# Performance work log

Measured on AMD Instinct MI355X. Metric: run time of the kernel, lower is better.

## Reference

```python
import jax, jax.numpy as jnp
from jax import lax
import numpy as np

GRID = 64
MAP = 15000.0
SCALE = MAP / GRID  # 234.375
R = int(1100 / SCALE)  # 4
SIGMA = 1.5
C = 16
B = 768
N_KILL = 49152
N_TRAIL = 393216

TOWERS = np.array([(8955, 8510), (9767, 10113), (11134, 11207), (11593, 11669), (13052, 12612), (12611, 13084), (5846, 6396), (5048, 4812), (3651, 3696), (3210, 3217), (2177, 1807), (1748, 2270), (4318, 13875), (981, 10441), (7943, 13411), (1512, 6699), (1169, 4287), (1172, 3583), (10481, 13650), (11275, 13657), (11275, 13663), (13866, 4505), (10504, 1029), (13327, 8226), (13624, 10572), (6919, 1483), (13599, 11319), (4281, 1253), (3468, 1230), (13594, 11319)], dtype=np.float32)

# ---- static buffers (numpy, computed once at import) ----
_tg = np.clip((TOWERS / SCALE).astype(np.int64), 0, GRID - 1)
TX, TY = _tg[:, 0], _tg[:, 1]
_xs = np.arange(GRID)
# per-tower coverage disc on the full canvas: equivalent to clipped range_mask placement
DISC = (((_xs[None, None, :] - TX[:, None, None]) ** 2 + (_xs[None, :, None] - TY[:, None, None]) ** 2) <= R * R).astype(np.float32)  # [30, H, W]
_ks = int(2 * 4 * SIGMA + 1)
if _ks % 2 == 0:
    _ks += 1
_x = (np.arange(_ks) - _ks // 2).astype(np.float32)
_k1 = np.exp(-_x ** 2 / (2 * SIGMA ** 2))
_k2 = np.outer(_k1, _k1)
_k2 = _k2 / _k2.sum()
KERNEL = np.broadcast_to(_k2, (C, 1, _ks, _ks)).astype(np.float32).copy()  # depthwise OIHW
PAD = _ks // 2
DRAG_X, DRAG_Y = int(10000.0 / SCALE), int(5000.0 / SCALE)   # (42, 21)
BARON_X, BARON_Y = int(5000.0 / SCALE), int(10000.0 / SCALE)  # (21, 42)


def _to_grid(coords):
    return jnp.clip((coords / SCALE).astype(jnp.int32), 0, GRID - 1)


def setup_inputs() -> dict:
    key = jax.random.key(0)
    ks = jax.random.split(key, 10)
    return {
        "player_coords": jax.random.uniform(ks[0], (N_TRAIL, 2), jnp.float32) * MAP,
        "player_vals": jax.random.uniform(ks[1], (N_TRAIL,), jnp.float32),
        "dead_towers_mask": jax.random.uniform(ks[2], (B, 30), jnp.float32),
        "kill_coords": jax.random.uniform(ks[3], (N_KILL, 2), jnp.float32) * MAP,
        "kill_vals": jax.random.uniform(ks[4], (N_KILL,), jnp.float32),
        "obj_status": jax.random.uniform(ks[5], (B, 2), jnp.float32),
        "player_b_idx": jax.random.randint(ks[6], (N_TRAIL,), 0, B, jnp.int32),
        "player_channels": jax.random.randint(ks[7], (N_TRAIL,), 0, 10, jnp.int32),
        "kill_teams": jax.random.randint(ks[8], (N_KILL,), 0, 2, jnp.int32),
        "kill_b_idx": jax.random.randint(ks[9], (N_KILL,), 0, B, jnp.int32),
    }


def reference(player_coords, player_vals, dead_towers_mask, kill_coords, kill_vals, obj_status, player_b_idx, player_channels, kill_teams, kill_b_idx):
    b = dead_towers_mask.shape[0]
    dead = dead_towers_mask > 0.5          # [B, 30]
    alive_f = (~dead).astype(jnp.float32)
    dead_f = dead.astype(jnp.float32)

    # channels 0/1: alive/dead tower markers (idempotent set -> scatter-max)
    ch0 = jnp.zeros((b, GRID, GRID), jnp.float32).at[:, TY, TX].max(alive_f)
    ch1 = jnp.zeros((b, GRID, GRID), jnp.float32).at[:, TY, TX].max(dead_f)

    # channel 2: max of binary range discs over alive towers == any-coverage indicator
    cov = alive_f @ jnp.asarray(DISC).reshape(30, -1)  # [B, H*W]
    ch2 = (cov > 0).astype(jnp.float32).reshape(b, GRID, GRID)

    # channel 3: objective markers
    ch3 = (jnp.zeros((b, GRID, GRID), jnp.float32)
           .at[:, DRAG_Y, DRAG_X].set((obj_status[:, 0] > 0.5).astype(jnp.float32))
           .at[:, BARON_Y, BARON_X].set((obj_status[:, 1] > 0.5).astype(jnp.float32)))

    canvas = jnp.concatenate(
        [ch0[:, None], ch1[:, None], ch2[:, None], ch3[:, None],
         jnp.zeros((b, C - 4, GRID, GRID), jnp.float32)], axis=1)  # [B, 16, H, W]

    # kill events: scatter-add into channels 4 + team
    kg = _to_grid(kill_coords)
    canvas = canvas.at[kill_b_idx, 4 + kill_teams, kg[:, 1], kg[:, 0]].add(kill_vals)

    # player trails: scatter-add into channels 6 + player_channel
    pg = _to_grid(player_coords)
    canvas = canvas.at[player_b_idx, 6 + player_channels, pg[:, 1], pg[:, 0]].add(player_vals)

    # depthwise gaussian blur
    blurred = lax.conv_general_dilated(
        canvas, jnp.asarray(KERNEL),
        window_strides=(1, 1), padding=[(PAD, PAD), (PAD, PAD)],
        feature_group_count=C,
        dimension_numbers=("NCHW", "OIHW", "NCHW"))
    return blurred
```

## Files before the change

### kernel.cpp

```cpp
#include <hip/hip_runtime.h>

#define GRID    64
#define BATCH   768
#define C       16
#define NT      30
#define N_KILL  49152
#define N_TRAIL 393216
#define CELLS   4096
#define IMG     (C * CELLS)
#define SCALE   234.375f
#define NBIN    (BATCH * 12)
#define STRIDE  65

__device__ constexpr int TX[NT] = {38,41,47,49,55,53,24,21,15,13, 9, 7,18, 4,33, 6, 4, 5,44,48,48,59,44,56,58,29,58,18,14,58};
__device__ constexpr int TY[NT] = {36,43,47,49,53,55,27,20,15,13, 7, 9,59,44,57,28,18,15,58,58,58,19, 4,35,45, 6,48, 5, 5,48};

__global__ __launch_bounds__(256) void zero_counts(unsigned* __restrict__ counts) {
    const int gid = blockIdx.x * 256 + threadIdx.x;
    if (gid < NBIN) counts[gid] = 0;
}

__global__ __launch_bounds__(256) void bin_points(
    const float* __restrict__ kc, const float* __restrict__ kv,
    const int*   __restrict__ kt, const int*   __restrict__ kb,
    const float* __restrict__ pc, const float* __restrict__ pv,
    const int*   __restrict__ pb, const int*   __restrict__ pch,
    unsigned* __restrict__ counts, uint2* __restrict__ recs, int cap)
{
    const int gid = blockIdx.x * 256 + threadIdx.x;
    int bin, cell; float val;
    if (gid < N_KILL) {
        const int i = gid;
        const int gx = min(max((int)(kc[2*i]   / SCALE), 0), GRID - 1);
        const int gy = min(max((int)(kc[2*i+1] / SCALE), 0), GRID - 1);
        cell = gy * GRID + gx;
        val  = kv[i];
        bin  = kb[i] * 12 + kt[i];
    } else {
        const int i = gid - N_KILL;
        const int gx = min(max((int)(pc[2*i]   / SCALE), 0), GRID - 1);
        const int gy = min(max((int)(pc[2*i+1] / SCALE), 0), GRID - 1);
        cell = gy * GRID + gx;
        val  = pv[i];
        bin  = pb[i] * 12 + 2 + pch[i];
    }
    const unsigned slot = atomicAdd(&counts[bin], 1u);
    if (slot < (unsigned)cap)
        recs[(size_t)bin * cap + slot] = make_uint2((unsigned)cell, __float_as_uint(val));
}

__global__ __launch_bounds__(256) void zero12(float* __restrict__ out) {
    const int j = blockIdx.x;
    const int b = j / 12, ch = 4 + j % 12;
    float4* p = (float4*)(out + (size_t)(b * C + ch) * CELLS);
    #pragma unroll
    for (int k = 0; k < 4; ++k) p[k * 256 + threadIdx.x] = make_float4(0.f,0.f,0.f,0.f);
}

__global__ __launch_bounds__(256) void scatter_global(
    const float* __restrict__ kc, const float* __restrict__ kv,
    const int*   __restrict__ kt, const int*   __restrict__ kb,
    const float* __restrict__ pc, const float* __restrict__ pv,
    const int*   __restrict__ pb, const int*   __restrict__ pch,
    float* __restrict__ out)
{
    const int gid = blockIdx.x * 256 + threadIdx.x;
    if (gid < N_KILL) {
        const int i = gid;
        const int gx = min(max((int)(kc[2*i]   / SCALE), 0), GRID - 1);
        const int gy = min(max((int)(kc[2*i+1] / SCALE), 0), GRID - 1);
        atomicAdd(out + (size_t)kb[i]*IMG + (4+kt[i])*CELLS + gy*GRID + gx, kv[i]);
    } else {
        const int i = gid - N_KILL;
        const int gx = min(max((int)(pc[2*i]   / SCALE), 0), GRID - 1);
        const int gy = min(max((int)(pc[2*i+1] / SCALE), 0), GRID - 1);
        atomicAdd(out + (size_t)pb[i]*IMG + (6+pch[i])*CELLS + gy*GRID + gx, pv[i]);
    }
}

template<bool BINS>
__global__ __launch_bounds__(64) void fused_blur(
    const float* __restrict__ dead_mask,
    const float* __restrict__ obj_status,
    const unsigned* __restrict__ counts,
    const uint2* __restrict__ recs, int cap,
    const float* __restrict__ canvas,
    float* __restrict__ out)
{
    const int t  = threadIdx.x;
    const int bc = blockIdx.x;
    const int b  = bc >> 4;
    const int c  = bc & 15;
    const size_t base = (size_t)bc * CELLS;

    __shared__ __align__(16) float s_buf[GRID * STRIDE];
    __shared__ float s_alive[NT];

    if (t < NT) s_alive[t] = (dead_mask[b * NT + t] > 0.5f) ? 0.0f : 1.0f;
    __syncthreads();

    float w[13];
    {
        float s = 0.0f;
        #pragma unroll
        for (int i = 0; i < 13; ++i) {
            const float d = (float)(i - 6);
            w[i] = expf(-d * d / 4.5f);
            s += w[i];
        }
        const float inv = 1.0f / s;
        #pragma unroll
        for (int i = 0; i < 13; ++i) w[i] *= inv;
    }

    float r[76];
    #pragma unroll
    for (int i = 0; i < 76; ++i) r[i] = 0.0f;

    if (c >= 4) {
        if (BINS) {
            float4 z = make_float4(0.f, 0.f, 0.f, 0.f);
            #pragma unroll
            for (int i = 0; i < 17; ++i) {
                const int idx = i * 64 + t;
                if (idx < (GRID * STRIDE) / 4) ((float4*)s_buf)[idx] = z;
            }
            __syncthreads();
            const int bin = b * 12 + (c - 4);
            const int n = min((int)counts[bin], cap);
            for (int i = t; i < n; i += 64) {
                const uint2 rec = recs[(size_t)bin * cap + i];
                atomicAdd(&s_buf[(rec.x >> 6) * STRIDE + (rec.x & 63)],
                          __uint_as_float(rec.y));
            }
            __syncthreads();
            #pragma unroll
            for (int k = 0; k < GRID; ++k) r[6 + k] = s_buf[t * STRIDE + k];
        } else {
            #pragma unroll
            for (int k = 0; k < 16; ++k) {
                const float4 v = ((const float4*)(canvas + base))[t * 16 + k];
                r[6 + 4*k + 0] = v.x; r[6 + 4*k + 1] = v.y;
                r[6 + 4*k + 2] = v.z; r[6 + 4*k + 3] = v.w;
            }
        }
    } else if (c == 0) {
        #pragma unroll
        for (int i = 0; i < NT; ++i)
            if (TY[i] == t) r[6 + TX[i]] = fmaxf(r[6 + TX[i]], s_alive[i]);
    } else if (c == 1) {
        #pragma unroll
        for (int i = 0; i < NT; ++i)
            if (TY[i] == t) r[6 + TX[i]] = fmaxf(r[6 + TX[i]], 1.0f - s_alive[i]);
    } else if (c == 2) {
        unsigned long long mask = 0ULL;
        #pragma unroll
        for (int i = 0; i < NT; ++i) {
            const int dy  = t - TY[i];
            const int ady = dy < 0 ? -dy : dy;
            if (ady <= 4 && s_alive[i] > 0.0f) {
                const int hw = (ady == 0) ? 4 : (ady <= 2) ? 3 : (ady == 3) ? 2 : 0;
                int lo = TX[i] - hw; if (lo < 0)  lo = 0;
                int hi = TX[i] + hw; if (hi > 63) hi = 63;
                mask |= (((1ULL << (hi - lo + 1)) - 1ULL) << lo);
            }
        }
        #pragma unroll
        for (int x = 0; x < GRID; ++x) r[6 + x] = (float)((mask >> x) & 1ULL);
    } else {
        const float o0 = obj_status[b * 2 + 0];
        const float o1 = obj_status[b * 2 + 1];
        if (t == 21) r[6 + 42] = (o0 > 0.5f) ? 1.0f : 0.0f;
        if (t == 42) r[6 + 21] = (o1 > 0.5f) ? 1.0f : 0.0f;
    }

    __syncthreads();

    #pragma unroll
    for (int x = 0; x < GRID; ++x) {
        float acc = 0.0f;
        #pragma unroll
        for (int d = 0; d < 13; ++d) acc = fmaf(w[d], r[x + d], acc);
        s_buf[x * STRIDE + t] = acc;
    }
    __syncthreads();

    float r2[76];
    #pragma unroll
    for (int i = 0; i < 76; ++i) r2[i] = 0.0f;
    #pragma unroll
    for (int k = 0; k < GRID; ++k) r2[6 + k] = s_buf[t * STRIDE + k];

    #pragma unroll
    for (int y = 0; y < GRID; ++y) {
        float acc = 0.0f;
        #pragma unroll
        for (int d = 0; d < 13; ++d) acc = fmaf(w[d], r2[y + d], acc);
        out[base + y * GRID + t] = acc;
    }
}

extern "C" void kernel_launch(void* const* d_in, const int* in_sizes, int n_in,
                              void* d_out, int out_size, void* d_ws, size_t ws_size,
                              hipStream_t stream)
{
    const float* player_coords = (const float*)d_in[0];
    const float* player_vals   = (const float*)d_in[1];
    const float* dead_mask     = (const float*)d_in[2];
    const float* kill_coords   = (const float*)d_in[3];
    const float* kill_vals     = (const float*)d_in[4];
    const float* obj_status    = (const float*)d_in[5];
    const int*   player_b      = (const int*)d_in[6];
    const int*   player_ch     = (const int*)d_in[7];
    const int*   kill_teams    = (const int*)d_in[8];
    const int*   kill_b        = (const int*)d_in[9];
    float* out = (float*)d_out;

    const size_t counts_bytes = (size_t)NBIN * sizeof(unsigned);
    size_t cap = 0;
    if (ws_size > counts_bytes)
        cap = (ws_size - counts_bytes) / ((size_t)NBIN * sizeof(uint2));
    if (cap > 256) cap = 256;

    const int n_scatter_blocks = (N_KILL + N_TRAIL) / 256;

    if (cap >= 128) {
        unsigned* counts = (unsigned*)d_ws;
        uint2*    recs   = (uint2*)((char*)d_ws + counts_bytes);
        zero_counts<<<(NBIN + 255) / 256, 256, 0, stream>>>(counts);
        bin_points<<<n_scatter_blocks, 256, 0, stream>>>(
            kill_coords, kill_vals, kill_teams, kill_b,
            player_coords, player_vals, player_b, player_ch,
            counts, recs, (int)cap);
        fused_blur<true><<<BATCH * C, 64, 0, stream>>>(
            dead_mask, obj_status, counts, recs, (int)cap, nullptr, out);
    } else {
        zero12<<<NBIN, 256, 0, stream>>>(out);
        scatter_global<<<n_scatter_blocks, 256, 0, stream>>>(
            kill_coords, kill_vals, kill_teams, kill_b,
            player_coords, player_vals, player_b, player_ch, out);
        fused_blur<false><<<BATCH * C, 64, 0, stream>>>(
            dead_mask, obj_status, nullptr, nullptr, 0, out, out);
    }
}
```

Measured before the change: 91.74 us.

## Bin points per image row and fuse horizontal blur into scatter

Points are now binned per (batch, channel, row) with a fixed capacity of 16 records, each storing only the x coordinate. Each thread then accumulates its row's horizontal 13-tap blur straight into shared memory. The old per-cell shared atomics and the separate horizontal pass go away. The scatter channels and the analytic channels (towers, coverage, objectives) now run in separate kernels. Both blur in two 32-column chunks with constant weights, which cuts shared memory and register use. In exchange, the workspace is much larger, and rows holding more than 16 points would be silently truncated.

```diff
diff --git a/kernel.cpp b/kernel.cpp
--- a/kernel.cpp
+++ b/kernel.cpp
@@ -9,15 +9,24 @@
 #define CELLS   4096
 #define IMG     (C * CELLS)
 #define SCALE   234.375f
-#define NBIN    (BATCH * 12)
-#define STRIDE  65
-
-__device__ constexpr int TX[NT] = {38,41,47,49,55,53,24,21,15,13, 9, 7,18, 4,33, 6, 4, 5,44,48,48,59,44,56,58,29,58,18,14,58};
-__device__ constexpr int TY[NT] = {36,43,47,49,53,55,27,20,15,13, 7, 9,59,44,57,28,18,15,58,58,58,19, 4,35,45, 6,48, 5, 5,48};
+#define NSC     12
+#define NSBIN   (BATCH * NSC)
+#define NRBIN   (NSBIN * GRID)
+#define CAP     16
+#define TRS     65
+#define TRN     2112
+
+__device__ constexpr int TXc[NT] = {38,41,47,49,55,53,24,21,15,13, 9, 7,18, 4,33, 6, 4, 5,44,48,48,59,44,56,58,29,58,18,14,58};
+__device__ constexpr int TYc[NT] = {36,43,47,49,53,55,27,20,15,13, 7, 9,59,44,57,28,18,15,58,58,58,19, 4,35,45, 6,48, 5, 5,48};
+
+__device__ constexpr float W13[13] = {
+    8.92216e-05f, 1.02820e-03f, 7.59741e-03f, 3.59943e-02f, 1.09341e-01f,
+    2.12968e-01f, 2.65964e-01f, 2.12968e-01f, 1.09341e-01f, 3.59943e-02f,
+    7.59741e-03f, 1.02820e-03f, 8.92216e-05f};
 
 __global__ __launch_bounds__(256) void zero_counts(unsigned* __restrict__ counts) {
     const int gid = blockIdx.x * 256 + threadIdx.x;
-    if (gid < NBIN) counts[gid] = 0;
+    if (gid < NRBIN) counts[gid] = 0;
 }
 
 __global__ __launch_bounds__(256) void bin_points(
@@ -25,33 +34,165 @@
     const int*   __restrict__ kt, const int*   __restrict__ kb,
     const float* __restrict__ pc, const float* __restrict__ pv,
     const int*   __restrict__ pb, const int*   __restrict__ pch,
-    unsigned* __restrict__ counts, uint2* __restrict__ recs, int cap)
+    unsigned* __restrict__ counts, uint2* __restrict__ recs)
 {
     const int gid = blockIdx.x * 256 + threadIdx.x;
-    int bin, cell; float val;
+    int rbin, gx; float val;
     if (gid < N_KILL) {
         const int i = gid;
-        const int gx = min(max((int)(kc[2*i]   / SCALE), 0), GRID - 1);
-        const int gy = min(max((int)(kc[2*i+1] / SCALE), 0), GRID - 1);
-        cell = gy * GRID + gx;
+        const float2 xy = ((const float2*)kc)[i];
+        gx = min(max((int)(xy.x / SCALE), 0), GRID - 1);
+        const int gy = min(max((int)(xy.y / SCALE), 0), GRID - 1);
         val  = kv[i];
-        bin  = kb[i] * 12 + kt[i];
+        rbin = (kb[i] * NSC + kt[i]) * GRID + gy;
     } else {
         const int i = gid - N_KILL;
-        const int gx = min(max((int)(pc[2*i]   / SCALE), 0), GRID - 1);
-        const int gy = min(max((int)(pc[2*i+1] / SCALE), 0), GRID - 1);
-        cell = gy * GRID + gx;
+        const float2 xy = ((const float2*)pc)[i];
+        gx = min(max((int)(xy.x / SCALE), 0), GRID - 1);
+        const int gy = min(max((int)(xy.y / SCALE), 0), GRID - 1);
         val  = pv[i];
-        bin  = pb[i] * 12 + 2 + pch[i];
-    }
-    const unsigned slot = atomicAdd(&counts[bin], 1u);
-    if (slot < (unsigned)cap)
-        recs[(size_t)bin * cap + slot] = make_uint2((unsigned)cell, __float_as_uint(val));
+        rbin = (pb[i] * NSC + 2 + pch[i]) * GRID + gy;
+    }
+    const unsigned slot = atomicAdd(&counts[rbin], 1u);
+    if (slot < CAP)
+        recs[(size_t)rbin * CAP + slot] = make_uint2((unsigned)gx, __float_as_uint(val));
+}
+
+__global__ __launch_bounds__(64) void blur_scatter(
+    const unsigned* __restrict__ counts,
+    const uint2* __restrict__ recs,
+    float* __restrict__ out)
+{
+    const int t = threadIdx.x;
+    const int j = blockIdx.x;
+    const int b = j / NSC, sc = j % NSC;
+    float* __restrict__ dst = out + ((size_t)b * C + 4 + sc) * CELLS;
+
+    __shared__ float s_tr[TRN];
+
+    const int rbin = j * GRID + t;
+    int n = (int)counts[rbin];
+    if (n > CAP) n = CAP;
+    const size_t rbase = (size_t)rbin * CAP;
+
+    for (int chunk = 0; chunk < 2; ++chunk) {
+        const int x0 = chunk * 32;
+        #pragma unroll
+        for (int i = 0; i < TRN / 64; ++i) s_tr[i * 64 + t] = 0.0f;
+        __syncthreads();
+
+        for (int i = 0; i < n; ++i) {
+            const uint2 rec = recs[rbase + i];
+            const int xp = (int)rec.x - 6 - x0;
+            const float v = __uint_as_float(rec.y);
+            #pragma unroll
+            for (int dd = 0; dd < 13; ++dd) {
+                const int xl = xp + dd;
+                if (xl >= 0 && xl < 32)
+                    s_tr[xl * TRS + t] += v * W13[dd];
+            }
+        }
+        __syncthreads();
+
+        const int ct = t & 31, rh = t >> 5;
+        float v44[44];
+        #pragma unroll
+        for (int k = 0; k < 44; ++k) {
+            const int row = rh * 32 + k - 6;
+            v44[k] = (row >= 0 && row < GRID) ? s_tr[ct * TRS + row] : 0.0f;
+        }
+        #pragma unroll
+        for (int yy = 0; yy < 32; ++yy) {
+            float acc = 0.0f;
+            #pragma unroll
+            for (int d = 0; d < 13; ++d) acc = fmaf(W13[d], v44[yy + d], acc);
+            dst[(rh * 32 + yy) * GRID + x0 + ct] = acc;
+        }
+        __syncthreads();
+    }
+}
+
+__global__ __launch_bounds__(64) void blur_analytic(
+    const float* __restrict__ dead_mask,
+    const float* __restrict__ obj_status,
+    float* __restrict__ out)
+{
+    const int t = threadIdx.x;
+    const int b = blockIdx.x >> 2;
+    const int c = blockIdx.x & 3;
+    float* __restrict__ dst = out + ((size_t)b * C + c) * CELLS;
+
+    __shared__ float s_tr[TRN];
+    __shared__ float s_alive[NT];
+    if (t < NT) s_alive[t] = (dead_mask[b * NT + t] > 0.5f) ? 0.0f : 1.0f;
+    __syncthreads();
+
+    float r[76];
+    #pragma unroll
+    for (int i = 0; i < 76; ++i) r[i] = 0.0f;
+
+    if (c == 0) {
+        #pragma unroll
+        for (int i = 0; i < NT; ++i)
+            if (TYc[i] == t) r[6 + TXc[i]] = fmaxf(r[6 + TXc[i]], s_alive[i]);
+    } else if (c == 1) {
+        #pragma unroll
+        for (int i = 0; i < NT; ++i)
+            if (TYc[i] == t) r[6 + TXc[i]] = fmaxf(r[6 + TXc[i]], 1.0f - s_alive[i]);
+    } else if (c == 2) {
+        unsigned long long mask = 0ULL;
+        #pragma unroll
+        for (int i = 0; i < NT; ++i) {
+            const int dy  = t - TYc[i];
+            const int ady = dy < 0 ? -dy : dy;
+            if (ady <= 4 && s_alive[i] > 0.0f) {
+                const int hw = (ady == 0) ? 4 : (ady <= 2) ? 3 : (ady == 3) ? 2 : 0;
+                int lo = TXc[i] - hw; if (lo < 0)  lo = 0;
+                int hi = TXc[i] + hw; if (hi > 63) hi = 63;
+                mask |= (((1ULL << (hi - lo + 1)) - 1ULL) << lo);
+            }
+        }
+        #pragma unroll
+        for (int x = 0; x < GRID; ++x) r[6 + x] = (float)((mask >> x) & 1ULL);
+    } else {
+        const float o0 = obj_status[b * 2 + 0];
+        const float o1 = obj_status[b * 2 + 1];
+        if (t == 21) r[6 + 42] = (o0 > 0.5f) ? 1.0f : 0.0f;
+        if (t == 42) r[6 + 21] = (o1 > 0.5f) ? 1.0f : 0.0f;
+    }
+
+    for (int chunk = 0; chunk < 2; ++chunk) {
+        const int x0 = chunk * 32;
+        #pragma unroll
+        for (int xl = 0; xl < 32; ++xl) {
+            float acc = 0.0f;
+            #pragma unroll
+            for (int d = 0; d < 13; ++d) acc = fmaf(W13[d], r[x0 + xl + d], acc);
+            s_tr[xl * TRS + t] = acc;
+        }
+        __syncthreads();
+
+        const int ct = t & 31, rh = t >> 5;
+        float v44[44];
+        #pragma unroll
+        for (int k = 0; k < 44; ++k) {
+            const int row = rh * 32 + k - 6;
+            v44[k] = (row >= 0 && row < GRID) ? s_tr[ct * TRS + row] : 0.0f;
+        }
+        #pragma unroll
+        for (int yy = 0; yy < 32; ++yy) {
+            float acc = 0.0f;
+            #pragma unroll
+            for (int d = 0; d < 13; ++d) acc = fmaf(W13[d], v44[yy + d], acc);
+            dst[(rh * 32 + yy) * GRID + x0 + ct] = acc;
+        }
+        __syncthreads();
+    }
 }
 
 __global__ __launch_bounds__(256) void zero12(float* __restrict__ out) {
     const int j = blockIdx.x;
-    const int b = j / 12, ch = 4 + j % 12;
+    const int b = j / NSC, ch = 4 + j % NSC;
     float4* p = (float4*)(out + (size_t)(b * C + ch) * CELLS);
     #pragma unroll
     for (int k = 0; k < 4; ++k) p[k * 256 + threadIdx.x] = make_float4(0.f,0.f,0.f,0.f);
@@ -78,125 +219,51 @@
     }
 }
 
-template<bool BINS>
-__global__ __launch_bounds__(64) void fused_blur(
-    const float* __restrict__ dead_mask,
-    const float* __restrict__ obj_status,
-    const unsigned* __restrict__ counts,
-    const uint2* __restrict__ recs, int cap,
-    const float* __restrict__ canvas,
-    float* __restrict__ out)
-{
-    const int t  = threadIdx.x;
-    const int bc = blockIdx.x;
-    const int b  = bc >> 4;
-    const int c  = bc & 15;
-    const size_t base = (size_t)bc * CELLS;
-
-    __shared__ __align__(16) float s_buf[GRID * STRIDE];
-    __shared__ float s_alive[NT];
-
-    if (t < NT) s_alive[t] = (dead_mask[b * NT + t] > 0.5f) ? 0.0f : 1.0f;
-    __syncthreads();
-
-    float w[13];
-    {
-        float s = 0.0f;
-        #pragma unroll
-        for (int i = 0; i < 13; ++i) {
-            const float d = (float)(i - 6);
-            w[i] = expf(-d * d / 4.5f);
-            s += w[i];
-        }
-        const float inv = 1.0f / s;
-        #pragma unroll
-        for (int i = 0; i < 13; ++i) w[i] *= inv;
-    }
+__global__ __launch_bounds__(64) void blur_scatter_fallback(float* __restrict__ out)
+{
+    const int t = threadIdx.x;
+    const int j = blockIdx.x;
+    const int b = j / NSC, sc = j % NSC;
+    float* __restrict__ dst = out + ((size_t)b * C + 4 + sc) * CELLS;
+
+    __shared__ float s_tr[TRN];
 
     float r[76];
     #pragma unroll
     for (int i = 0; i < 76; ++i) r[i] = 0.0f;
-
-    if (c >= 4) {
-        if (BINS) {
-            float4 z = make_float4(0.f, 0.f, 0.f, 0.f);
-            #pragma unroll
-            for (int i = 0; i < 17; ++i) {
-                const int idx = i * 64 + t;
-                if (idx < (GRID * STRIDE) / 4) ((float4*)s_buf)[idx] = z;
-            }
-            __syncthreads();
-            const int bin = b * 12 + (c - 4);
-            const int n = min((int)counts[bin], cap);
-            for (int i = t; i < n; i += 64) {
-                const uint2 rec = recs[(size_t)bin * cap + i];
-                atomicAdd(&s_buf[(rec.x >> 6) * STRIDE + (rec.x & 63)],
-                          __uint_as_float(rec.y));
-            }
-            __syncthreads();
-            #pragma unroll
-            for (int k = 0; k < GRID; ++k) r[6 + k] = s_buf[t * STRIDE + k];
-        } else {
-            #pragma unroll
-            for (int k = 0; k < 16; ++k) {
-                const float4 v = ((const float4*)(canvas + base))[t * 16 + k];
-                r[6 + 4*k + 0] = v.x; r[6 + 4*k + 1] = v.y;
-                r[6 + 4*k + 2] = v.z; r[6 + 4*k + 3] = v.w;
-            }
-        }
-    } else if (c == 0) {
-        #pragma unroll
-        for (int i = 0; i < NT; ++i)
-            if (TY[i] == t) r[6 + TX[i]] = fmaxf(r[6 + TX[i]], s_alive[i]);
-    } else if (c == 1) {
-        #pragma unroll
-        for (int i = 0; i < NT; ++i)
-            if (TY[i] == t) r[6 + TX[i]] = fmaxf(r[6 + TX[i]], 1.0f - s_alive[i]);
-    } else if (c == 2) {
-        unsigned long long mask = 0ULL;
-        #pragma unroll
-        for (int i = 0; i < NT; ++i) {
-            const int dy  = t - TY[i];
-            const int ady = dy < 0 ? -dy : dy;
-            if (ady <= 4 && s_alive[i] > 0.0f) {
-                const int hw = (ady == 0) ? 4 : (ady <= 2) ? 3 : (ady == 3) ? 2 : 0;
-                int lo = TX[i] - hw; if (lo < 0)  lo = 0;
-                int hi = TX[i] + hw; if (hi > 63) hi = 63;
-                mask |= (((1ULL << (hi - lo + 1)) - 1ULL) << lo);
-            }
-        }
-        #pragma unroll
-        for (int x = 0; x < GRID; ++x) r[6 + x] = (float)((mask >> x) & 1ULL);
-    } else {
-        const float o0 = obj_status[b * 2 + 0];
-        const float o1 = obj_status[b * 2 + 1];
-        if (t == 21) r[6 + 42] = (o0 > 0.5f) ? 1.0f : 0.0f;
-        if (t == 42) r[6 + 21] = (o1 > 0.5f) ? 1.0f : 0.0f;
-    }
-
+    #pragma unroll
+    for (int k = 0; k < 16; ++k) {
+        const float4 v = ((const float4*)dst)[t * 16 + k];
+        r[6 + 4*k + 0] = v.x; r[6 + 4*k + 1] = v.y;
+        r[6 + 4*k + 2] = v.z; r[6 + 4*k + 3] = v.w;
+    }
     __syncthreads();
 
-    #pragma unroll
-    for (int x = 0; x < GRID; ++x) {
-        float acc = 0.0f;
-        #pragma unroll
-        for (int d = 0; d < 13; ++d) acc = fmaf(w[d], r[x + d], acc);
-        s_buf[x * STRIDE + t] = acc;
-    }
-    __syncthreads();
-
-    float r2[76];
-    #pragma unroll
-    for (int i = 0; i < 76; ++i) r2[i] = 0.0f;
-    #pragma unroll
-    for (int k = 0; k < GRID; ++k) r2[6 + k] = s_buf[t * STRIDE + k];
-
-    #pragma unroll
-    for (int y = 0; y < GRID; ++y) {
-        float acc = 0.0f;
-        #pragma unroll
-        for (int d = 0; d < 13; ++d) acc = fmaf(w[d], r2[y + d], acc);
-        out[base + y * GRID + t] = acc;
+    for (int chunk = 0; chunk < 2; ++chunk) {
+        const int x0 = chunk * 32;
+        #pragma unroll
+        for (int xl = 0; xl < 32; ++xl) {
+            float acc = 0.0f;
+            #pragma unroll
+            for (int d = 0; d < 13; ++d) acc = fmaf(W13[d], r[x0 + xl + d], acc);
+            s_tr[xl * TRS + t] = acc;
+        }
+        __syncthreads();
+        const int ct = t & 31, rh = t >> 5;
+        float v44[44];
+        #pragma unroll
+        for (int k = 0; k < 44; ++k) {
+            const int row = rh * 32 + k - 6;
+            v44[k] = (row >= 0 && row < GRID) ? s_tr[ct * TRS + row] : 0.0f;
+        }
+        #pragma unroll
+        for (int yy = 0; yy < 32; ++yy) {
+            float acc = 0.0f;
+            #pragma unroll
+            for (int d = 0; d < 13; ++d) acc = fmaf(W13[d], v44[yy + d], acc);
+            dst[(rh * 32 + yy) * GRID + x0 + ct] = acc;
+        }
+        __syncthreads();
     }
 }
 
@@ -216,30 +283,26 @@
     const int*   kill_b        = (const int*)d_in[9];
     float* out = (float*)d_out;
 
-    const size_t counts_bytes = (size_t)NBIN * sizeof(unsigned);
-    size_t cap = 0;
-    if (ws_size > counts_bytes)
-        cap = (ws_size - counts_bytes) / ((size_t)NBIN * sizeof(uint2));
-    if (cap > 256) cap = 256;
-
+    const size_t counts_bytes = (size_t)NRBIN * sizeof(unsigned);
+    const size_t recs_bytes   = (size_t)NRBIN * CAP * sizeof(uint2);
     const int n_scatter_blocks = (N_KILL + N_TRAIL) / 256;
 
-    if (cap >= 128) {
+    if (ws_size >= counts_bytes + recs_bytes) {
         unsigned* counts = (unsigned*)d_ws;
         uint2*    recs   = (uint2*)((char*)d_ws + counts_bytes);
-        zero_counts<<<(NBIN + 255) / 256, 256, 0, stream>>>(counts);
+        zero_counts<<<(NRBIN + 255) / 256, 256, 0, stream>>>(counts);
         bin_points<<<n_scatter_blocks, 256, 0, stream>>>(
             kill_coords, kill_vals, kill_teams, kill_b,
             player_coords, player_vals, player_b, player_ch,
-            counts, recs, (int)cap);
-        fused_blur<true><<<BATCH * C, 64, 0, stream>>>(
-            dead_mask, obj_status, counts, recs, (int)cap, nullptr, out);
+            counts, recs);
+        blur_scatter<<<NSBIN, 64, 0, stream>>>(counts, recs, out);
+        blur_analytic<<<BATCH * 4, 64, 0, stream>>>(dead_mask, obj_status, out);
     } else {
-        zero12<<<NBIN, 256, 0, stream>>>(out);
+        zero12<<<NSBIN, 256, 0, stream>>>(out);
         scatter_global<<<n_scatter_blocks, 256, 0, stream>>>(
             kill_coords, kill_vals, kill_teams, kill_b,
             player_coords, player_vals, player_b, player_ch, out);
-        fused_blur<false><<<BATCH * C, 64, 0, stream>>>(
-            dead_mask, obj_status, nullptr, nullptr, 0, out, out);
-    }
-}
+        blur_scatter_fallback<<<NSBIN, 64, 0, stream>>>(out);
+        blur_analytic<<<BATCH * 4, 64, 0, stream>>>(dead_mask, obj_status, out);
+    }
+}
```

Result: slower. 122.0 us (+33.0%).

## Splat horizontal blur taps directly from binned points into transposed shared tile

Applied to the files above, without the earlier changes.

For the scattered channels, each binned point now contributes its 13 weighted horizontal taps via shared-memory atomics directly into a transposed tile, replacing the dense horizontal convolution pass. Gaussian weights become compile-time constants instead of per-thread expf, and the transposed tile uses a padded stride allowing float4 column reads. This trades 64x13 FMAs per row for point-proportional atomics, and the fixed 128-record capacity could drop points if a bin overflows.

```diff
diff --git a/kernel.cpp b/kernel.cpp
--- a/kernel.cpp
+++ b/kernel.cpp
@@ -9,15 +9,22 @@
 #define CELLS   4096
 #define IMG     (C * CELLS)
 #define SCALE   234.375f
-#define NBIN    (BATCH * 12)
-#define STRIDE  65
-
-__device__ constexpr int TX[NT] = {38,41,47,49,55,53,24,21,15,13, 9, 7,18, 4,33, 6, 4, 5,44,48,48,59,44,56,58,29,58,18,14,58};
-__device__ constexpr int TY[NT] = {36,43,47,49,53,55,27,20,15,13, 7, 9,59,44,57,28,18,15,58,58,58,19, 4,35,45, 6,48, 5, 5,48};
+#define NSC     12
+#define NIMG    (BATCH * NSC)
+#define CAPI    128
+#define STR     68
+
+__device__ constexpr int TXc[NT] = {38,41,47,49,55,53,24,21,15,13, 9, 7,18, 4,33, 6, 4, 5,44,48,48,59,44,56,58,29,58,18,14,58};
+__device__ constexpr int TYc[NT] = {36,43,47,49,53,55,27,20,15,13, 7, 9,59,44,57,28,18,15,58,58,58,19, 4,35,45, 6,48, 5, 5,48};
+
+__device__ constexpr float W13[13] = {
+    8.92216e-05f, 1.02820e-03f, 7.59741e-03f, 3.59943e-02f, 1.09341e-01f,
+    2.12968e-01f, 2.65964e-01f, 2.12968e-01f, 1.09341e-01f, 3.59943e-02f,
+    7.59741e-03f, 1.02820e-03f, 8.92216e-05f};
 
 __global__ __launch_bounds__(256) void zero_counts(unsigned* __restrict__ counts) {
     const int gid = blockIdx.x * 256 + threadIdx.x;
-    if (gid < NBIN) counts[gid] = 0;
+    if (gid < NIMG) counts[gid] = 0;
 }
 
 __global__ __launch_bounds__(256) void bin_points(
@@ -25,33 +32,153 @@
     const int*   __restrict__ kt, const int*   __restrict__ kb,
     const float* __restrict__ pc, const float* __restrict__ pv,
     const int*   __restrict__ pb, const int*   __restrict__ pch,
-    unsigned* __restrict__ counts, uint2* __restrict__ recs, int cap)
+    unsigned* __restrict__ counts, uint2* __restrict__ recs)
 {
     const int gid = blockIdx.x * 256 + threadIdx.x;
-    int bin, cell; float val;
+    int img, gx, gy; float val;
     if (gid < N_KILL) {
         const int i = gid;
-        const int gx = min(max((int)(kc[2*i]   / SCALE), 0), GRID - 1);
-        const int gy = min(max((int)(kc[2*i+1] / SCALE), 0), GRID - 1);
-        cell = gy * GRID + gx;
-        val  = kv[i];
-        bin  = kb[i] * 12 + kt[i];
+        const float2 xy = ((const float2*)kc)[i];
+        gx = min(max((int)(xy.x / SCALE), 0), GRID - 1);
+        gy = min(max((int)(xy.y / SCALE), 0), GRID - 1);
+        val = kv[i];
+        img = kb[i] * NSC + kt[i];
     } else {
         const int i = gid - N_KILL;
-        const int gx = min(max((int)(pc[2*i]   / SCALE), 0), GRID - 1);
-        const int gy = min(max((int)(pc[2*i+1] / SCALE), 0), GRID - 1);
-        cell = gy * GRID + gx;
-        val  = pv[i];
-        bin  = pb[i] * 12 + 2 + pch[i];
-    }
-    const unsigned slot = atomicAdd(&counts[bin], 1u);
-    if (slot < (unsigned)cap)
-        recs[(size_t)bin * cap + slot] = make_uint2((unsigned)cell, __float_as_uint(val));
+        const float2 xy = ((const float2*)pc)[i];
+        gx = min(max((int)(xy.x / SCALE), 0), GRID - 1);
+        gy = min(max((int)(xy.y / SCALE), 0), GRID - 1);
+        val = pv[i];
+        img = pb[i] * NSC + 2 + pch[i];
+    }
+    const unsigned slot = atomicAdd(&counts[img], 1u);
+    if (slot < CAPI)
+        recs[(size_t)img * CAPI + slot] =
+            make_uint2((unsigned)(gx | (gy << 8)), __float_as_uint(val));
+}
+
+template<bool BINS>
+__global__ __launch_bounds__(64) void fused_blur(
+    const float* __restrict__ dead_mask,
+    const float* __restrict__ obj_status,
+    const unsigned* __restrict__ counts,
+    const uint2* __restrict__ recs,
+    const float* canvas,
+    float* out)
+{
+    const int t  = threadIdx.x;
+    const int bc = blockIdx.x;
+    const int b  = bc >> 4;
+    const int c  = bc & 15;
+    const size_t base = (size_t)bc * CELLS;
+
+    __shared__ __align__(16) float s_tr[GRID * STR];
+    __shared__ float s_alive[NT];
+
+    if (c < 4 && t < NT) s_alive[t] = (dead_mask[b * NT + t] > 0.5f) ? 0.0f : 1.0f;
+
+    if (BINS && c >= 4) {
+        const float4 z = make_float4(0.f, 0.f, 0.f, 0.f);
+        #pragma unroll
+        for (int i = 0; i < 17; ++i) ((float4*)s_tr)[i * 64 + t] = z;
+        __syncthreads();
+
+        const int img = b * NSC + (c - 4);
+        int n = (int)counts[img];
+        if (n > CAPI) n = CAPI;
+        const size_t ibase = (size_t)img * CAPI;
+        const float wlane = W13[t % 13];
+        const int ntaps = n * 13;
+
+        for (int k0 = 0; k0 < ntaps; k0 += 64) {
+            const int k = k0 + t;
+            const unsigned i  = (unsigned)k / 13u;
+            const int      dd = k - (int)i * 13;
+            const uint2 rec = recs[ibase + min((int)i, n - 1)];
+            const int gx = (int)(rec.x & 0xFFu);
+            const int gy = (int)(rec.x >> 8);
+            const int xl = gx - 6 + dd;
+            const float w = __shfl(wlane, dd);
+            if (k < ntaps && (unsigned)xl < 64u)
+                atomicAdd(&s_tr[xl * STR + gy], __uint_as_float(rec.y) * w);
+        }
+        __syncthreads();
+    } else {
+        if (c < 4) __syncthreads();
+
+        float r[76];
+        #pragma unroll
+        for (int i = 0; i < 76; ++i) r[i] = 0.0f;
+
+        if (c == 0) {
+            #pragma unroll
+            for (int i = 0; i < NT; ++i)
+                if (TYc[i] == t) r[6 + TXc[i]] = fmaxf(r[6 + TXc[i]], s_alive[i]);
+        } else if (c == 1) {
+            #pragma unroll
+            for (int i = 0; i < NT; ++i)
+                if (TYc[i] == t) r[6 + TXc[i]] = fmaxf(r[6 + TXc[i]], 1.0f - s_alive[i]);
+        } else if (c == 2) {
+            unsigned long long mask = 0ULL;
+            #pragma unroll
+            for (int i = 0; i < NT; ++i) {
+                const int dy  = t - TYc[i];
+                const int ady = dy < 0 ? -dy : dy;
+                if (ady <= 4 && s_alive[i] > 0.0f) {
+                    const int hw = (ady == 0) ? 4 : (ady <= 2) ? 3 : (ady == 3) ? 2 : 0;
+                    int lo = TXc[i] - hw; if (lo < 0)  lo = 0;
+                    int hi = TXc[i] + hw; if (hi > 63) hi = 63;
+                    mask |= (((1ULL << (hi - lo + 1)) - 1ULL) << lo);
+                }
+            }
+            #pragma unroll
+            for (int x = 0; x < GRID; ++x) r[6 + x] = (float)((mask >> x) & 1ULL);
+        } else if (c == 3) {
+            const float o0 = obj_status[b * 2 + 0];
+            const float o1 = obj_status[b * 2 + 1];
+            if (t == 21) r[6 + 42] = (o0 > 0.5f) ? 1.0f : 0.0f;
+            if (t == 42) r[6 + 21] = (o1 > 0.5f) ? 1.0f : 0.0f;
+        } else {
+            #pragma unroll
+            for (int k = 0; k < 16; ++k) {
+                const float4 v = ((const float4*)(canvas + base))[t * 16 + k];
+                r[6 + 4*k + 0] = v.x; r[6 + 4*k + 1] = v.y;
+                r[6 + 4*k + 2] = v.z; r[6 + 4*k + 3] = v.w;
+            }
+        }
+
+        #pragma unroll
+        for (int x = 0; x < GRID; ++x) {
+            float acc = 0.0f;
+            #pragma unroll
+            for (int d = 0; d < 13; ++d) acc = fmaf(W13[d], r[x + d], acc);
+            s_tr[x * STR + t] = acc;
+        }
+        __syncthreads();
+    }
+
+    float v[76];
+    #pragma unroll
+    for (int i = 0; i < 6; ++i) { v[i] = 0.0f; v[70 + i] = 0.0f; }
+    const float4* col = (const float4*)(s_tr + t * STR);
+    #pragma unroll
+    for (int k = 0; k < 16; ++k) {
+        const float4 q = col[k];
+        v[6 + 4*k + 0] = q.x; v[6 + 4*k + 1] = q.y;
+        v[6 + 4*k + 2] = q.z; v[6 + 4*k + 3] = q.w;
+    }
+    #pragma unroll
+    for (int y = 0; y < GRID; ++y) {
+        float acc = 0.0f;
+        #pragma unroll
+        for (int d = 0; d < 13; ++d) acc = fmaf(W13[d], v[y + d], acc);
+        out[base + y * GRID + t] = acc;
+    }
 }
 
 __global__ __launch_bounds__(256) void zero12(float* __restrict__ out) {
     const int j = blockIdx.x;
-    const int b = j / 12, ch = 4 + j % 12;
+    const int b = j / NSC, ch = 4 + j % NSC;
     float4* p = (float4*)(out + (size_t)(b * C + ch) * CELLS);
     #pragma unroll
     for (int k = 0; k < 4; ++k) p[k * 256 + threadIdx.x] = make_float4(0.f,0.f,0.f,0.f);
@@ -75,128 +202,6 @@
         const int gx = min(max((int)(pc[2*i]   / SCALE), 0), GRID - 1);
         const int gy = min(max((int)(pc[2*i+1] / SCALE), 0), GRID - 1);
         atomicAdd(out + (size_t)pb[i]*IMG + (6+pch[i])*CELLS + gy*GRID + gx, pv[i]);
-    }
-}
-
-template<bool BINS>
-__global__ __launch_bounds__(64) void fused_blur(
-    const float* __restrict__ dead_mask,
-    const float* __restrict__ obj_status,
-    const unsigned* __restrict__ counts,
-    const uint2* __restrict__ recs, int cap,
-    const float* __restrict__ canvas,
-    float* __restrict__ out)
-{
-    const int t  = threadIdx.x;
-    const int bc = blockIdx.x;
-    const int b  = bc >> 4;
-    const int c  = bc & 15;
-    const size_t base = (size_t)bc * CELLS;
-
-    __shared__ __align__(16) float s_buf[GRID * STRIDE];
-    __shared__ float s_alive[NT];
-
-    if (t < NT) s_alive[t] = (dead_mask[b * NT + t] > 0.5f) ? 0.0f : 1.0f;
-    __syncthreads();
-
-    float w[13];
-    {
-        float s = 0.0f;
-        #pragma unroll
-        for (int i = 0; i < 13; ++i) {
-            const float d = (float)(i - 6);
-            w[i] = expf(-d * d / 4.5f);
-            s += w[i];
-        }
-        const float inv = 1.0f / s;
-        #pragma unroll
-        for (int i = 0; i < 13; ++i) w[i] *= inv;
-    }
-
-    float r[76];
-    #pragma unroll
-    for (int i = 0; i < 76; ++i) r[i] = 0.0f;
-
-    if (c >= 4) {
-        if (BINS) {
-            float4 z = make_float4(0.f, 0.f, 0.f, 0.f);
-            #pragma unroll
-            for (int i = 0; i < 17; ++i) {
-                const int idx = i * 64 + t;
-                if (idx < (GRID * STRIDE) / 4) ((float4*)s_buf)[idx] = z;
-            }
-            __syncthreads();
-            const int bin = b * 12 + (c - 4);
-            const int n = min((int)counts[bin], cap);
-            for (int i = t; i < n; i += 64) {
-                const uint2 rec = recs[(size_t)bin * cap + i];
-                atomicAdd(&s_buf[(rec.x >> 6) * STRIDE + (rec.x & 63)],
-                          __uint_as_float(rec.y));
-            }
-            __syncthreads();
-            #pragma unroll
-            for (int k = 0; k < GRID; ++k) r[6 + k] = s_buf[t * STRIDE + k];
-        } else {
-            #pragma unroll
-            for (int k = 0; k < 16; ++k) {
-                const float4 v = ((const float4*)(canvas + base))[t * 16 + k];
-                r[6 + 4*k + 0] = v.x; r[6 + 4*k + 1] = v.y;
-                r[6 + 4*k + 2] = v.z; r[6 + 4*k + 3] = v.w;
-            }
-        }
-    } else if (c == 0) {
-        #pragma unroll
-        for (int i = 0; i < NT; ++i)
-            if (TY[i] == t) r[6 + TX[i]] = fmaxf(r[6 + TX[i]], s_alive[i]);
-    } else if (c == 1) {
-        #pragma unroll
-        for (int i = 0; i < NT; ++i)
-            if (TY[i] == t) r[6 + TX[i]] = fmaxf(r[6 + TX[i]], 1.0f - s_alive[i]);
-    } else if (c == 2) {
-        unsigned long long mask = 0ULL;
-        #pragma unroll
-        for (int i = 0; i < NT; ++i) {
-            const int dy  = t - TY[i];
-            const int ady = dy < 0 ? -dy : dy;
-            if (ady <= 4 && s_alive[i] > 0.0f) {
-                const int hw = (ady == 0) ? 4 : (ady <= 2) ? 3 : (ady == 3) ? 2 : 0;
-                int lo = TX[i] - hw; if (lo < 0)  lo = 0;
-                int hi = TX[i] + hw; if (hi > 63) hi = 63;
-                mask |= (((1ULL << (hi - lo + 1)) - 1ULL) << lo);
-            }
-        }
-        #pragma unroll
-        for (int x = 0; x < GRID; ++x) r[6 + x] = (float)((mask >> x) & 1ULL);
-    } else {
-        const float o0 = obj_status[b * 2 + 0];
-        const float o1 = obj_status[b * 2 + 1];
-        if (t == 21) r[6 + 42] = (o0 > 0.5f) ? 1.0f : 0.0f;
-        if (t == 42) r[6 + 21] = (o1 > 0.5f) ? 1.0f : 0.0f;
-    }
-
-    __syncthreads();
-
-    #pragma unroll
-    for (int x = 0; x < GRID; ++x) {
-        float acc = 0.0f;
-        #pragma unroll
-        for (int d = 0; d < 13; ++d) acc = fmaf(w[d], r[x + d], acc);
-        s_buf[x * STRIDE + t] = acc;
-    }
-    __syncthreads();
-
-    float r2[76];
-    #pragma unroll
-    for (int i = 0; i < 76; ++i) r2[i] = 0.0f;
-    #pragma unroll
-    for (int k = 0; k < GRID; ++k) r2[6 + k] = s_buf[t * STRIDE + k];
-
-    #pragma unroll
-    for (int y = 0; y < GRID; ++y) {
-        float acc = 0.0f;
-        #pragma unroll
-        for (int d = 0; d < 13; ++d) acc = fmaf(w[d], r2[y + d], acc);
-        out[base + y * GRID + t] = acc;
     }
 }
 
@@ -216,30 +221,26 @@
     const int*   kill_b        = (const int*)d_in[9];
     float* out = (float*)d_out;
 
-    const size_t counts_bytes = (size_t)NBIN * sizeof(unsigned);
-    size_t cap = 0;
-    if (ws_size > counts_bytes)
-        cap = (ws_size - counts_bytes) / ((size_t)NBIN * sizeof(uint2));
-    if (cap > 256) cap = 256;
-
+    const size_t counts_bytes = (size_t)NIMG * sizeof(unsigned);
+    const size_t recs_bytes   = (size_t)NIMG * CAPI * sizeof(uint2);
     const int n_scatter_blocks = (N_KILL + N_TRAIL) / 256;
 
-    if (cap >= 128) {
+    if (ws_size >= counts_bytes + recs_bytes) {
         unsigned* counts = (unsigned*)d_ws;
         uint2*    recs   = (uint2*)((char*)d_ws + counts_bytes);
-        zero_counts<<<(NBIN + 255) / 256, 256, 0, stream>>>(counts);
+        zero_counts<<<(NIMG + 255) / 256, 256, 0, stream>>>(counts);
         bin_points<<<n_scatter_blocks, 256, 0, stream>>>(
             kill_coords, kill_vals, kill_teams, kill_b,
             player_coords, player_vals, player_b, player_ch,
-            counts, recs, (int)cap);
+            counts, recs);
         fused_blur<true><<<BATCH * C, 64, 0, stream>>>(
-            dead_mask, obj_status, counts, recs, (int)cap, nullptr, out);
-    } else {
-        zero12<<<NBIN, 256, 0, stream>>>(out);
+            dead_mask, obj_status, counts, recs, nullptr, out);
+    } else {
+        zero12<<<NIMG, 256, 0, stream>>>(out);
         scatter_global<<<n_scatter_blocks, 256, 0, stream>>>(
             kill_coords, kill_vals, kill_teams, kill_b,
             player_coords, player_vals, player_b, player_ch, out);
         fused_blur<false><<<BATCH * C, 64, 0, stream>>>(
-            dead_mask, obj_status, nullptr, nullptr, 0, out, out);
-    }
-}
+            dead_mask, obj_status, nullptr, nullptr, out, out);
+    }
+}
```

Result: slower. 102.9 us (+12.1%).
